# Optimization experiments

Hardware: AMD Instinct MI355X
Metric: run time of the kernel (lower is better)

The kernel has to match this reference:

```python
import jax, jax.numpy as jnp
import numpy as np

B, L, D = 2, 2048, 2048
NH, HD = 16, 128
SCALE = HD ** -0.5


def setup_inputs() -> dict:
    key = jax.random.key(0)
    ks = jax.random.split(key, 9)
    s = D ** -0.5  # roughly torch Linear init scale
    return {
        "hidden_states": jax.random.normal(ks[0], (B, L, D), dtype=jnp.float32),
        "Wq": jax.random.normal(ks[1], (NH * HD, D), dtype=jnp.float32) * s,
        "bq": jnp.zeros((NH * HD,), dtype=jnp.float32),
        "Wk": jax.random.normal(ks[2], (NH * HD, D), dtype=jnp.float32) * s,
        "bk": jnp.zeros((NH * HD,), dtype=jnp.float32),
        "Wv": jax.random.normal(ks[3], (NH * HD, D), dtype=jnp.float32) * s,
        "bv": jnp.zeros((NH * HD,), dtype=jnp.float32),
        "Wo": jax.random.normal(ks[4], (D, NH * HD), dtype=jnp.float32) * s,
        "bo": jnp.zeros((D,), dtype=jnp.float32),
    }


def reference(hidden_states, Wq, bq, Wk, bk, Wv, bv, Wo, bo):
    # projections (torch Linear: x @ W.T + b), split into heads: b s h d
    q = (hidden_states @ Wq.T + bq).reshape(B, L, NH, HD)
    k = (hidden_states @ Wk.T + bk).reshape(B, L, NH, HD)
    v = (hidden_states @ Wv.T + bv).reshape(B, L, NH, HD)
    # scores: [B, NH, L, L]
    scores = jnp.einsum("bqhd,bkhd->bhqk", q, k) * SCALE
    causal = jnp.tril(jnp.ones((L, L), dtype=bool))  # True = keep
    scores = jnp.where(causal, scores, jnp.float32(-jnp.inf))
    probs = jax.nn.softmax(scores, axis=-1)
    out = jnp.einsum("bhqk,bkhd->bqhd", probs, v).reshape(B, L, NH * HD)
    return out @ Wo.T + bo
```

## Files before the change

### kernel.cpp

```cpp
#include <hip/hip_runtime.h>

#define B_  2
#define L_  2048
#define D_  2048
#define NH_ 16
#define HD_ 128

typedef __bf16 bf16_t;
typedef __bf16 bf16x8 __attribute__((ext_vector_type(8)));
typedef __bf16 bf16x4 __attribute__((ext_vector_type(4)));
typedef float  f32x4  __attribute__((ext_vector_type(4)));

typedef const __attribute__((address_space(1))) void* gas_ptr;
typedef __attribute__((address_space(3))) void* las_ptr;

__device__ __forceinline__ void g2l16(const void* g, void* l) {
    __builtin_amdgcn_global_load_lds((gas_ptr)g, (las_ptr)l, 16, 0, 0);
}

__device__ __forceinline__ void raw_barrier() {
    asm volatile("s_barrier" ::: "memory");
}
__device__ __forceinline__ void wait_vm8() {
    asm volatile("s_waitcnt vmcnt(8)" ::: "memory");
}
__device__ __forceinline__ void wait_vm0() {
    asm volatile("s_waitcnt vmcnt(0)" ::: "memory");
}

__global__ __launch_bounds__(256) void cvt_all(const float* __restrict__ X,
                                               const float* __restrict__ Wq,
                                               const float* __restrict__ Wk,
                                               const float* __restrict__ Wv,
                                               const float* __restrict__ Wo,
                                               bf16_t* __restrict__ Xb,
                                               bf16_t* __restrict__ Wqkvb,
                                               bf16_t* __restrict__ Wob) {
    int i = blockIdx.x * 256 + threadIdx.x;
    const float* src;
    bf16_t* dst;
    int off;
    if (i < 2097152) { src = X; dst = Xb; off = i; }
    else {
        int j = i - 2097152;
        int w = j >> 20;
        off = j & 1048575;
        src = (w == 0) ? Wq : (w == 1) ? Wk : (w == 2) ? Wv : Wo;
        dst = (w == 3) ? Wob : Wqkvb + (size_t)w * 4194304;
    }
    float4 v = ((const float4*)src)[off];
    bf16x4 o;
    o[0] = (bf16_t)v.x; o[1] = (bf16_t)v.y; o[2] = (bf16_t)v.z; o[3] = (bf16_t)v.w;
    ((bf16x4*)dst)[off] = o;
}

template <bool BF16OUT>
__global__ __launch_bounds__(256) void gemm_bt(const bf16_t* __restrict__ A,
                                               const bf16_t* __restrict__ Bw,
                                               const float* __restrict__ bias,
                                               void* __restrict__ C,
                                               int M, int N, int K) {
    constexpr int BK = 32;
    __shared__ bf16_t Al[128 * BK];
    __shared__ bf16_t Bl[128 * BK];
    const int tid  = threadIdx.x;
    const int wave = tid >> 6, lane = tid & 63;
    const int quad = lane >> 4, l16 = lane & 15;
    const int tm = blockIdx.y * 128, tn = blockIdx.x * 128;
    const int wm = (wave >> 1) * 64, wn = (wave & 1) * 64;

    const int srow = wave * 16 + (lane >> 2);
    const int scol = (lane & 3) * 8;
    const bf16_t* Ag = A  + (size_t)(tm + srow) * K + scol;
    const bf16_t* Bg = Bw + (size_t)(tn + srow) * K + scol;
    const size_t rowskip = (size_t)64 * K;
    bf16_t* Al0 = Al + (wave * 16) * BK;
    bf16_t* Al1 = Al + (64 + wave * 16) * BK;
    bf16_t* Bl0 = Bl + (wave * 16) * BK;
    bf16_t* Bl1 = Bl + (64 + wave * 16) * BK;

    f32x4 acc[4][4] = {};

    for (int k0 = 0; k0 < K; k0 += BK) {
        g2l16(Ag + k0, Al0);
        g2l16(Ag + k0 + rowskip, Al1);
        g2l16(Bg + k0, Bl0);
        g2l16(Bg + k0 + rowskip, Bl1);
        __syncthreads();

        bf16x8 af[4], bf[4];
#pragma unroll
        for (int i = 0; i < 4; ++i)
            af[i] = *(const bf16x8*)(Al + (wm + i * 16 + l16) * BK + quad * 8);
#pragma unroll
        for (int j = 0; j < 4; ++j)
            bf[j] = *(const bf16x8*)(Bl + (wn + j * 16 + l16) * BK + quad * 8);
#pragma unroll
        for (int i = 0; i < 4; ++i)
#pragma unroll
            for (int j = 0; j < 4; ++j)
                acc[i][j] = __builtin_amdgcn_mfma_f32_16x16x32_bf16(af[i], bf[j], acc[i][j], 0, 0, 0);
        __syncthreads();
    }

#pragma unroll
    for (int j = 0; j < 4; ++j) {
        const int col = tn + wn + j * 16 + l16;
        const float bv = bias[col];
#pragma unroll
        for (int i = 0; i < 4; ++i) {
            const int row0 = tm + wm + i * 16 + quad * 4;
#pragma unroll
            for (int r = 0; r < 4; ++r) {
                float v = acc[i][j][r] + bv;
                if (BF16OUT)
                    ((bf16_t*)C)[(size_t)(row0 + r) * N + col] = (bf16_t)v;
                else
                    ((float*)C)[(size_t)(row0 + r) * N + col] = v;
            }
        }
    }
}

__global__ __launch_bounds__(256) void gemm_qkv(const bf16_t* __restrict__ A,
                                                const bf16_t* __restrict__ Bw,
                                                const float* __restrict__ b0,
                                                const float* __restrict__ b1,
                                                const float* __restrict__ b2,
                                                bf16_t* __restrict__ C,
                                                int M, int N, int K) {
    constexpr int BK = 32;
    __shared__ bf16_t Al[128 * BK];
    __shared__ bf16_t Bl[128 * BK];
    const int tid  = threadIdx.x;
    const int wave = tid >> 6, lane = tid & 63;
    const int quad = lane >> 4, l16 = lane & 15;
    const int tm = blockIdx.y * 128, tn = blockIdx.x * 128;
    const int wm = (wave >> 1) * 64, wn = (wave & 1) * 64;

    const int seg = tn >> 11;
    const float* bias = (seg == 0) ? b0 : (seg == 1) ? b1 : b2;

    const int srow = wave * 16 + (lane >> 2);
    const int scol = (lane & 3) * 8;
    const bf16_t* Ag = A  + (size_t)(tm + srow) * K + scol;
    const bf16_t* Bg = Bw + (size_t)(tn + srow) * K + scol;
    const size_t rowskip = (size_t)64 * K;
    bf16_t* Al0 = Al + (wave * 16) * BK;
    bf16_t* Al1 = Al + (64 + wave * 16) * BK;
    bf16_t* Bl0 = Bl + (wave * 16) * BK;
    bf16_t* Bl1 = Bl + (64 + wave * 16) * BK;

    f32x4 acc[4][4] = {};

    for (int k0 = 0; k0 < K; k0 += BK) {
        g2l16(Ag + k0, Al0);
        g2l16(Ag + k0 + rowskip, Al1);
        g2l16(Bg + k0, Bl0);
        g2l16(Bg + k0 + rowskip, Bl1);
        __syncthreads();

        bf16x8 af[4], bf[4];
#pragma unroll
        for (int i = 0; i < 4; ++i)
            af[i] = *(const bf16x8*)(Al + (wm + i * 16 + l16) * BK + quad * 8);
#pragma unroll
        for (int j = 0; j < 4; ++j)
            bf[j] = *(const bf16x8*)(Bl + (wn + j * 16 + l16) * BK + quad * 8);
#pragma unroll
        for (int i = 0; i < 4; ++i)
#pragma unroll
            for (int j = 0; j < 4; ++j)
                acc[i][j] = __builtin_amdgcn_mfma_f32_16x16x32_bf16(af[i], bf[j], acc[i][j], 0, 0, 0);
        __syncthreads();
    }

#pragma unroll
    for (int j = 0; j < 4; ++j) {
        const int col = tn + wn + j * 16 + l16;
        const float bv = bias[col & 2047];
#pragma unroll
        for (int i = 0; i < 4; ++i) {
            const int row0 = tm + wm + i * 16 + quad * 4;
#pragma unroll
            for (int r = 0; r < 4; ++r)
                C[(size_t)(row0 + r) * N + col] = (bf16_t)(acc[i][j][r] + bv);
        }
    }
}

__global__ __launch_bounds__(256) void transpose_v(const bf16_t* __restrict__ QKV,
                                                   bf16_t* __restrict__ Vt) {
    __shared__ bf16_t t[64 * 136];
    const int tid = threadIdx.x;
    const int tt = blockIdx.x;
    const int bh = blockIdx.y;
    const int b = bh >> 4, h = bh & 15;
#pragma unroll
    for (int c = 0; c < 8; ++c) {
        int chunk = c * 256 + tid;
        int tok = chunk >> 5;
        int dof = (chunk & 31) * 4;
        bf16x4 v = *(const bf16x4*)(QKV + (size_t)(b * L_ + tt * 64 + tok) * 6144 + 4096 + h * HD_ + dof);
        *(bf16x4*)(&t[tok * 136 + dof]) = v;
    }
    __syncthreads();
#pragma unroll
    for (int c = 0; c < 4; ++c) {
        int chunk = c * 256 + tid;
        int d = chunk >> 3;
        int tof = (chunk & 7) * 8;
        bf16x8 v;
#pragma unroll
        for (int j = 0; j < 8; ++j) v[j] = t[(tof + j) * 136 + d];
        *(bf16x8*)(Vt + (size_t)(bh * HD_ + d) * L_ + tt * 64 + tof) = v;
    }
}

__global__ __launch_bounds__(256, 2) void attn_kernel(const bf16_t* __restrict__ QKV,
                                                      const bf16_t* __restrict__ Vt,
                                                      bf16_t* __restrict__ Ctx) {
    constexpr float SCALE = 0.08838834764831845f;
    constexpr float MFIX  = 8.0f;
    const int bid = blockIdx.x;
    const int bh = bid & 31;
    const int qt = 15 - (bid >> 5);
    const int b = bh >> 4, h = bh & 15;
    const int tid = threadIdx.x, wave = tid >> 6, lane = tid & 63;
    const int quad = lane >> 4, l16 = lane & 15;
    const int q0 = qt * 128;

    __shared__ bf16_t Kl[2][64 * 128];
    __shared__ bf16_t Vl[2][128 * 64];
    __shared__ bf16_t Pl[4][16 * 72];

    bf16x8 qf[2][4];
#pragma unroll
    for (int s = 0; s < 2; ++s) {
        const bf16_t* qp = QKV + (size_t)(b * L_ + q0 + wave * 32 + s * 16 + l16) * 6144 + h * HD_ + quad * 8;
#pragma unroll
        for (int ks = 0; ks < 4; ++ks) qf[s][ks] = *(const bf16x8*)(qp + ks * 32);
    }

    bf16x8 ones;
#pragma unroll
    for (int j = 0; j < 8; ++j) ones[j] = (bf16_t)1.0f;

    f32x4 oacc[2][8] = {};
    f32x4 lacc[2] = {};

    const bf16_t* Kg = QKV + (size_t)(b * L_) * 6144 + 2048 + h * HD_;
    const bf16_t* Vg = Vt + (size_t)(bh * HD_) * L_;

    auto stage = [&](int tile, int p) {
        const bf16_t* kg = Kg + (size_t)tile * 64 * 6144;
        const bf16_t* vg = Vg + tile * 64;
#pragma unroll
        for (int c = 0; c < 4; ++c) {
            int row = c * 16 + wave * 4 + (lane >> 4);
            int gcol = ((lane & 15) ^ (row & 15)) * 8;
            g2l16(kg + (size_t)row * 6144 + gcol, &Kl[p][(c * 16 + wave * 4) * 128]);
        }
#pragma unroll
        for (int c = 0; c < 4; ++c) {
            int row = c * 32 + wave * 8 + (lane >> 3);
            int gcol = ((lane & 7) ^ (row & 7)) * 8;
            g2l16(vg + (size_t)row * L_ + gcol, &Vl[p][(c * 32 + wave * 8) * 64]);
        }
    };

    const int n = 2 * qt + 2;
    stage(0, 0);

    for (int it = 0; it < n; ++it) {
        const int p = it & 1;
        if (it + 1 < n) {
            stage(it + 1, p ^ 1);
            wait_vm8();
        } else {
            wait_vm0();
        }
        raw_barrier();

        const int kb = it * 64;
        const bool need_mask = (it >= n - 2);

        f32x4 sa[2][4] = {};
#pragma unroll
        for (int nt = 0; nt < 4; ++nt) {
            const int krow = nt * 16 + l16;
#pragma unroll
            for (int ks = 0; ks < 4; ++ks) {
                bf16x8 kf = *(const bf16x8*)(&Kl[p][krow * 128 + (((ks * 4 + quad) ^ l16) * 8)]);
                sa[0][nt] = __builtin_amdgcn_mfma_f32_16x16x32_bf16(qf[0][ks], kf, sa[0][nt], 0, 0, 0);
                sa[1][nt] = __builtin_amdgcn_mfma_f32_16x16x32_bf16(qf[1][ks], kf, sa[1][nt], 0, 0, 0);
            }
        }

        bf16x8 pf0[2], pf1[2];
#pragma unroll
        for (int nt = 0; nt < 4; ++nt)
#pragma unroll
            for (int r = 0; r < 4; ++r) {
                float sv = sa[0][nt][r] * SCALE - MFIX;
                if (need_mask) {
                    const int key = kb + nt * 16 + l16;
                    const int qq = q0 + wave * 32 + quad * 4 + r;
                    sv = (key <= qq) ? sv : -1e30f;
                }
                Pl[wave][(quad * 4 + r) * 72 + nt * 16 + l16] = (bf16_t)__expf(sv);
            }
        pf0[0] = *(const bf16x8*)(&Pl[wave][l16 * 72 + quad * 8]);
        pf0[1] = *(const bf16x8*)(&Pl[wave][l16 * 72 + 32 + quad * 8]);

#pragma unroll
        for (int nt = 0; nt < 4; ++nt)
#pragma unroll
            for (int r = 0; r < 4; ++r) {
                float sv = sa[1][nt][r] * SCALE - MFIX;
                if (need_mask) {
                    const int key = kb + nt * 16 + l16;
                    const int qq = q0 + wave * 32 + 16 + quad * 4 + r;
                    sv = (key <= qq) ? sv : -1e30f;
                }
                Pl[wave][(quad * 4 + r) * 72 + nt * 16 + l16] = (bf16_t)__expf(sv);
            }
        pf1[0] = *(const bf16x8*)(&Pl[wave][l16 * 72 + quad * 8]);
        pf1[1] = *(const bf16x8*)(&Pl[wave][l16 * 72 + 32 + quad * 8]);

        lacc[0] = __builtin_amdgcn_mfma_f32_16x16x32_bf16(pf0[0], ones, lacc[0], 0, 0, 0);
        lacc[0] = __builtin_amdgcn_mfma_f32_16x16x32_bf16(pf0[1], ones, lacc[0], 0, 0, 0);
        lacc[1] = __builtin_amdgcn_mfma_f32_16x16x32_bf16(pf1[0], ones, lacc[1], 0, 0, 0);
        lacc[1] = __builtin_amdgcn_mfma_f32_16x16x32_bf16(pf1[1], ones, lacc[1], 0, 0, 0);

#pragma unroll
        for (int dt = 0; dt < 8; ++dt) {
            const int drow = dt * 16 + l16;
#pragma unroll
            for (int ks = 0; ks < 2; ++ks) {
                bf16x8 vf = *(const bf16x8*)(&Vl[p][drow * 64 + (((ks * 4 + quad) ^ (drow & 7)) * 8)]);
                oacc[0][dt] = __builtin_amdgcn_mfma_f32_16x16x32_bf16(pf0[ks], vf, oacc[0][dt], 0, 0, 0);
                oacc[1][dt] = __builtin_amdgcn_mfma_f32_16x16x32_bf16(pf1[ks], vf, oacc[1][dt], 0, 0, 0);
            }
        }
        raw_barrier();
    }

#pragma unroll
    for (int s = 0; s < 2; ++s)
#pragma unroll
        for (int r = 0; r < 4; ++r) {
            const float inv = 1.0f / lacc[s][r];
            const int q = q0 + wave * 32 + s * 16 + quad * 4 + r;
            bf16_t* cp = Ctx + (size_t)(b * L_ + q) * 2048 + h * HD_;
#pragma unroll
            for (int dt = 0; dt < 8; ++dt)
                cp[dt * 16 + l16] = (bf16_t)(oacc[s][dt][r] * inv);
        }
}

extern "C" void kernel_launch(void* const* d_in, const int* in_sizes, int n_in,
                              void* d_out, int out_size, void* d_ws, size_t ws_size,
                              hipStream_t stream) {
    const float* X  = (const float*)d_in[0];
    const float* Wq = (const float*)d_in[1];
    const float* bq = (const float*)d_in[2];
    const float* Wk = (const float*)d_in[3];
    const float* bk = (const float*)d_in[4];
    const float* Wv = (const float*)d_in[5];
    const float* bv = (const float*)d_in[6];
    const float* Wo = (const float*)d_in[7];
    const float* bo = (const float*)d_in[8];
    float* out = (float*)d_out;

    char* ws = (char*)d_ws;
    bf16_t* Xb   = (bf16_t*)(ws);
    bf16_t* Vtb  = (bf16_t*)(ws);
    bf16_t* Wqkv = (bf16_t*)(ws + 16777216);
    bf16_t* Ctx  = (bf16_t*)(ws + 16777216);
    bf16_t* Wob  = (bf16_t*)(ws + 41943040);
    bf16_t* QKV  = (bf16_t*)(ws + 50331648);

    cvt_all<<<24576, 256, 0, stream>>>(X, Wq, Wk, Wv, Wo, Xb, Wqkv, Wob);

    gemm_qkv<<<dim3(48, 32), 256, 0, stream>>>(Xb, Wqkv, bq, bk, bv, QKV,
                                               B_ * L_, 3 * D_, D_);

    transpose_v<<<dim3(L_ / 64, B_ * NH_), 256, 0, stream>>>(QKV, Vtb);
    attn_kernel<<<dim3(512), 256, 0, stream>>>(QKV, Vtb, Ctx);

    gemm_bt<false><<<dim3(16, 32), 256, 0, stream>>>(Ctx, Wob, bo, out,
                                                     B_ * L_, D_, D_);
}
```

Measured before the change: 409.2 us.

## Double-buffer GEMM LDS loads and fuse V transpose into QKV GEMM epilogue

Both GEMM kernels now use a two-stage LDS buffer. The next K-tile's global-to-LDS loads are issued before computing the current one, with vmcnt waits and raw barriers replacing the per-iteration syncthreads, so memory latency is meant to overlap with MFMA work. The QKV GEMM's V-segment blocks write a transposed V through a swizzled LDS tile straight into the Vt layout, which removes the separate transpose kernel and its extra pass over V. Q and K now go to a narrower 4096-wide buffer, and the workspace layout changes to match. The trade-off is doubled LDS use, which may lower occupancy.

```diff
diff --git a/kernel.cpp b/kernel.cpp
--- a/kernel.cpp
+++ b/kernel.cpp
@@ -23,6 +23,9 @@
 }
 __device__ __forceinline__ void wait_vm8() {
     asm volatile("s_waitcnt vmcnt(8)" ::: "memory");
+}
+__device__ __forceinline__ void wait_vm4() {
+    asm volatile("s_waitcnt vmcnt(4)" ::: "memory");
 }
 __device__ __forceinline__ void wait_vm0() {
     asm volatile("s_waitcnt vmcnt(0)" ::: "memory");
@@ -54,15 +57,13 @@
     ((bf16x4*)dst)[off] = o;
 }
 
-template <bool BF16OUT>
 __global__ __launch_bounds__(256) void gemm_bt(const bf16_t* __restrict__ A,
                                                const bf16_t* __restrict__ Bw,
                                                const float* __restrict__ bias,
-                                               void* __restrict__ C,
+                                               float* __restrict__ C,
                                                int M, int N, int K) {
     constexpr int BK = 32;
-    __shared__ bf16_t Al[128 * BK];
-    __shared__ bf16_t Bl[128 * BK];
+    __shared__ __align__(16) bf16_t smem[16384];
     const int tid  = threadIdx.x;
     const int wave = tid >> 6, lane = tid & 63;
     const int quad = lane >> 4, l16 = lane & 15;
@@ -74,33 +75,41 @@
     const bf16_t* Ag = A  + (size_t)(tm + srow) * K + scol;
     const bf16_t* Bg = Bw + (size_t)(tn + srow) * K + scol;
     const size_t rowskip = (size_t)64 * K;
-    bf16_t* Al0 = Al + (wave * 16) * BK;
-    bf16_t* Al1 = Al + (64 + wave * 16) * BK;
-    bf16_t* Bl0 = Bl + (wave * 16) * BK;
-    bf16_t* Bl1 = Bl + (64 + wave * 16) * BK;
+
+    auto stage = [&](int k0, int p) {
+        bf16_t* a = smem + p * 4096 + (wave * 16) * BK;
+        bf16_t* bl = smem + 8192 + p * 4096 + (wave * 16) * BK;
+        g2l16(Ag + k0, a);
+        g2l16(Ag + k0 + rowskip, a + 64 * BK);
+        g2l16(Bg + k0, bl);
+        g2l16(Bg + k0 + rowskip, bl + 64 * BK);
+    };
 
     f32x4 acc[4][4] = {};
-
-    for (int k0 = 0; k0 < K; k0 += BK) {
-        g2l16(Ag + k0, Al0);
-        g2l16(Ag + k0 + rowskip, Al1);
-        g2l16(Bg + k0, Bl0);
-        g2l16(Bg + k0 + rowskip, Bl1);
-        __syncthreads();
-
+    const int niter = K / BK;
+    stage(0, 0);
+
+    for (int i = 0; i < niter; ++i) {
+        const int p = i & 1;
+        if (i + 1 < niter) { stage((i + 1) * BK, p ^ 1); wait_vm4(); }
+        else wait_vm0();
+        raw_barrier();
+
+        const bf16_t* Alp = smem + p * 4096;
+        const bf16_t* Blp = smem + 8192 + p * 4096;
         bf16x8 af[4], bf[4];
 #pragma unroll
-        for (int i = 0; i < 4; ++i)
-            af[i] = *(const bf16x8*)(Al + (wm + i * 16 + l16) * BK + quad * 8);
+        for (int ii = 0; ii < 4; ++ii)
+            af[ii] = *(const bf16x8*)(Alp + (wm + ii * 16 + l16) * BK + quad * 8);
 #pragma unroll
         for (int j = 0; j < 4; ++j)
-            bf[j] = *(const bf16x8*)(Bl + (wn + j * 16 + l16) * BK + quad * 8);
-#pragma unroll
-        for (int i = 0; i < 4; ++i)
+            bf[j] = *(const bf16x8*)(Blp + (wn + j * 16 + l16) * BK + quad * 8);
+#pragma unroll
+        for (int ii = 0; ii < 4; ++ii)
 #pragma unroll
             for (int j = 0; j < 4; ++j)
-                acc[i][j] = __builtin_amdgcn_mfma_f32_16x16x32_bf16(af[i], bf[j], acc[i][j], 0, 0, 0);
-        __syncthreads();
+                acc[ii][j] = __builtin_amdgcn_mfma_f32_16x16x32_bf16(af[ii], bf[j], acc[ii][j], 0, 0, 0);
+        raw_barrier();
     }
 
 #pragma unroll
@@ -111,13 +120,8 @@
         for (int i = 0; i < 4; ++i) {
             const int row0 = tm + wm + i * 16 + quad * 4;
 #pragma unroll
-            for (int r = 0; r < 4; ++r) {
-                float v = acc[i][j][r] + bv;
-                if (BF16OUT)
-                    ((bf16_t*)C)[(size_t)(row0 + r) * N + col] = (bf16_t)v;
-                else
-                    ((float*)C)[(size_t)(row0 + r) * N + col] = v;
-            }
+            for (int r = 0; r < 4; ++r)
+                C[(size_t)(row0 + r) * N + col] = acc[i][j][r] + bv;
         }
     }
 }
@@ -127,11 +131,10 @@
                                                 const float* __restrict__ b0,
                                                 const float* __restrict__ b1,
                                                 const float* __restrict__ b2,
-                                                bf16_t* __restrict__ C,
-                                                int M, int N, int K) {
-    constexpr int BK = 32;
-    __shared__ bf16_t Al[128 * BK];
-    __shared__ bf16_t Bl[128 * BK];
+                                                bf16_t* __restrict__ QK,
+                                                bf16_t* __restrict__ Vt) {
+    constexpr int BK = 32, K = D_;
+    __shared__ __align__(16) bf16_t smem[17408];
     const int tid  = threadIdx.x;
     const int wave = tid >> 6, lane = tid & 63;
     const int quad = lane >> 4, l16 = lane & 15;
@@ -146,78 +149,87 @@
     const bf16_t* Ag = A  + (size_t)(tm + srow) * K + scol;
     const bf16_t* Bg = Bw + (size_t)(tn + srow) * K + scol;
     const size_t rowskip = (size_t)64 * K;
-    bf16_t* Al0 = Al + (wave * 16) * BK;
-    bf16_t* Al1 = Al + (64 + wave * 16) * BK;
-    bf16_t* Bl0 = Bl + (wave * 16) * BK;
-    bf16_t* Bl1 = Bl + (64 + wave * 16) * BK;
+
+    auto stage = [&](int k0, int p) {
+        bf16_t* a = smem + p * 4096 + (wave * 16) * BK;
+        bf16_t* bl = smem + 8192 + p * 4096 + (wave * 16) * BK;
+        g2l16(Ag + k0, a);
+        g2l16(Ag + k0 + rowskip, a + 64 * BK);
+        g2l16(Bg + k0, bl);
+        g2l16(Bg + k0 + rowskip, bl + 64 * BK);
+    };
 
     f32x4 acc[4][4] = {};
-
-    for (int k0 = 0; k0 < K; k0 += BK) {
-        g2l16(Ag + k0, Al0);
-        g2l16(Ag + k0 + rowskip, Al1);
-        g2l16(Bg + k0, Bl0);
-        g2l16(Bg + k0 + rowskip, Bl1);
+    const int niter = K / BK;
+    stage(0, 0);
+
+    for (int i = 0; i < niter; ++i) {
+        const int p = i & 1;
+        if (i + 1 < niter) { stage((i + 1) * BK, p ^ 1); wait_vm4(); }
+        else wait_vm0();
+        raw_barrier();
+
+        const bf16_t* Alp = smem + p * 4096;
+        const bf16_t* Blp = smem + 8192 + p * 4096;
+        bf16x8 af[4], bf[4];
+#pragma unroll
+        for (int ii = 0; ii < 4; ++ii)
+            af[ii] = *(const bf16x8*)(Alp + (wm + ii * 16 + l16) * BK + quad * 8);
+#pragma unroll
+        for (int j = 0; j < 4; ++j)
+            bf[j] = *(const bf16x8*)(Blp + (wn + j * 16 + l16) * BK + quad * 8);
+#pragma unroll
+        for (int ii = 0; ii < 4; ++ii)
+#pragma unroll
+            for (int j = 0; j < 4; ++j)
+                acc[ii][j] = __builtin_amdgcn_mfma_f32_16x16x32_bf16(af[ii], bf[j], acc[ii][j], 0, 0, 0);
+        raw_barrier();
+    }
+
+    if (seg < 2) {
+#pragma unroll
+        for (int j = 0; j < 4; ++j) {
+            const int col = tn + wn + j * 16 + l16;
+            const float bv = bias[col & 2047];
+#pragma unroll
+            for (int i = 0; i < 4; ++i) {
+                const int row0 = tm + wm + i * 16 + quad * 4;
+#pragma unroll
+                for (int r = 0; r < 4; ++r)
+                    QK[(size_t)(row0 + r) * 4096 + col] = (bf16_t)(acc[i][j][r] + bv);
+            }
+        }
+    } else {
+        const int h = (tn >> 7) - 32;
+        const int b = tm >> 11;
+        const int tokbase = tm & 2047;
         __syncthreads();
-
-        bf16x8 af[4], bf[4];
-#pragma unroll
-        for (int i = 0; i < 4; ++i)
-            af[i] = *(const bf16x8*)(Al + (wm + i * 16 + l16) * BK + quad * 8);
-#pragma unroll
-        for (int j = 0; j < 4; ++j)
-            bf[j] = *(const bf16x8*)(Bl + (wn + j * 16 + l16) * BK + quad * 8);
-#pragma unroll
-        for (int i = 0; i < 4; ++i)
-#pragma unroll
-            for (int j = 0; j < 4; ++j)
-                acc[i][j] = __builtin_amdgcn_mfma_f32_16x16x32_bf16(af[i], bf[j], acc[i][j], 0, 0, 0);
+#pragma unroll
+        for (int j = 0; j < 4; ++j) {
+            const int d = wn + j * 16 + l16;
+            const float bv = bias[(tn + wn + j * 16 + l16) & 2047];
+#pragma unroll
+            for (int i = 0; i < 4; ++i)
+#pragma unroll
+                for (int r = 0; r < 4; ++r) {
+                    const int tok = wm + i * 16 + quad * 4 + r;
+                    smem[d * 136 + (((tok >> 3) ^ (d & 7)) << 3) + (tok & 7)] =
+                        (bf16_t)(acc[i][j][r] + bv);
+                }
+        }
         __syncthreads();
-    }
-
-#pragma unroll
-    for (int j = 0; j < 4; ++j) {
-        const int col = tn + wn + j * 16 + l16;
-        const float bv = bias[col & 2047];
-#pragma unroll
-        for (int i = 0; i < 4; ++i) {
-            const int row0 = tm + wm + i * 16 + quad * 4;
-#pragma unroll
-            for (int r = 0; r < 4; ++r)
-                C[(size_t)(row0 + r) * N + col] = (bf16_t)(acc[i][j][r] + bv);
-        }
-    }
-}
-
-__global__ __launch_bounds__(256) void transpose_v(const bf16_t* __restrict__ QKV,
-                                                   bf16_t* __restrict__ Vt) {
-    __shared__ bf16_t t[64 * 136];
-    const int tid = threadIdx.x;
-    const int tt = blockIdx.x;
-    const int bh = blockIdx.y;
-    const int b = bh >> 4, h = bh & 15;
-#pragma unroll
-    for (int c = 0; c < 8; ++c) {
-        int chunk = c * 256 + tid;
-        int tok = chunk >> 5;
-        int dof = (chunk & 31) * 4;
-        bf16x4 v = *(const bf16x4*)(QKV + (size_t)(b * L_ + tt * 64 + tok) * 6144 + 4096 + h * HD_ + dof);
-        *(bf16x4*)(&t[tok * 136 + dof]) = v;
-    }
-    __syncthreads();
-#pragma unroll
-    for (int c = 0; c < 4; ++c) {
-        int chunk = c * 256 + tid;
-        int d = chunk >> 3;
-        int tof = (chunk & 7) * 8;
-        bf16x8 v;
-#pragma unroll
-        for (int j = 0; j < 8; ++j) v[j] = t[(tof + j) * 136 + d];
-        *(bf16x8*)(Vt + (size_t)(bh * HD_ + d) * L_ + tt * 64 + tof) = v;
-    }
-}
-
-__global__ __launch_bounds__(256, 2) void attn_kernel(const bf16_t* __restrict__ QKV,
+        const int d = tid >> 1, half = tid & 1;
+        bf16_t* gp = Vt + ((size_t)(b * NH_ + h) * HD_ + d) * L_ + tokbase + half * 64;
+#pragma unroll
+        for (int c2 = 0; c2 < 8; ++c2) {
+            const int cc = half * 8 + c2;
+            bf16x8 v = *(const bf16x8*)(smem + d * 136 + ((cc ^ (d & 7)) << 3));
+            *(bf16x8*)(gp + c2 * 8) = v;
+        }
+    }
+}
+
+__global__ __launch_bounds__(256, 2) void attn_kernel(const bf16_t* __restrict__ QK,
                                                       const bf16_t* __restrict__ Vt,
                                                       bf16_t* __restrict__ Ctx) {
     constexpr float SCALE = 0.08838834764831845f;
@@ -237,7 +249,7 @@
     bf16x8 qf[2][4];
 #pragma unroll
     for (int s = 0; s < 2; ++s) {
-        const bf16_t* qp = QKV + (size_t)(b * L_ + q0 + wave * 32 + s * 16 + l16) * 6144 + h * HD_ + quad * 8;
+        const bf16_t* qp = QK + (size_t)(b * L_ + q0 + wave * 32 + s * 16 + l16) * 4096 + h * HD_ + quad * 8;
 #pragma unroll
         for (int ks = 0; ks < 4; ++ks) qf[s][ks] = *(const bf16x8*)(qp + ks * 32);
     }
@@ -249,17 +261,17 @@
     f32x4 oacc[2][8] = {};
     f32x4 lacc[2] = {};
 
-    const bf16_t* Kg = QKV + (size_t)(b * L_) * 6144 + 2048 + h * HD_;
+    const bf16_t* Kg = QK + (size_t)(b * L_) * 4096 + 2048 + h * HD_;
     const bf16_t* Vg = Vt + (size_t)(bh * HD_) * L_;
 
     auto stage = [&](int tile, int p) {
-        const bf16_t* kg = Kg + (size_t)tile * 64 * 6144;
+        const bf16_t* kg = Kg + (size_t)tile * 64 * 4096;
         const bf16_t* vg = Vg + tile * 64;
 #pragma unroll
         for (int c = 0; c < 4; ++c) {
             int row = c * 16 + wave * 4 + (lane >> 4);
             int gcol = ((lane & 15) ^ (row & 15)) * 8;
-            g2l16(kg + (size_t)row * 6144 + gcol, &Kl[p][(c * 16 + wave * 4) * 128]);
+            g2l16(kg + (size_t)row * 4096 + gcol, &Kl[p][(c * 16 + wave * 4) * 128]);
         }
 #pragma unroll
         for (int c = 0; c < 4; ++c) {
@@ -375,20 +387,18 @@
 
     char* ws = (char*)d_ws;
     bf16_t* Xb   = (bf16_t*)(ws);
-    bf16_t* Vtb  = (bf16_t*)(ws);
+    bf16_t* Ctx  = (bf16_t*)(ws);
     bf16_t* Wqkv = (bf16_t*)(ws + 16777216);
-    bf16_t* Ctx  = (bf16_t*)(ws + 16777216);
     bf16_t* Wob  = (bf16_t*)(ws + 41943040);
-    bf16_t* QKV  = (bf16_t*)(ws + 50331648);
+    bf16_t* QKb  = (bf16_t*)(ws + 50331648);
+    bf16_t* Vtb  = (bf16_t*)(ws + 83886080);
 
     cvt_all<<<24576, 256, 0, stream>>>(X, Wq, Wk, Wv, Wo, Xb, Wqkv, Wob);
 
-    gemm_qkv<<<dim3(48, 32), 256, 0, stream>>>(Xb, Wqkv, bq, bk, bv, QKV,
-                                               B_ * L_, 3 * D_, D_);
-
-    transpose_v<<<dim3(L_ / 64, B_ * NH_), 256, 0, stream>>>(QKV, Vtb);
-    attn_kernel<<<dim3(512), 256, 0, stream>>>(QKV, Vtb, Ctx);
-
-    gemm_bt<false><<<dim3(16, 32), 256, 0, stream>>>(Ctx, Wob, bo, out,
-                                                     B_ * L_, D_, D_);
-}
+    gemm_qkv<<<dim3(48, 32), 256, 0, stream>>>(Xb, Wqkv, bq, bk, bv, QKb, Vtb);
+
+    attn_kernel<<<dim3(512), 256, 0, stream>>>(QKb, Vtb, Ctx);
+
+    gemm_bt<<<dim3(16, 32), 256, 0, stream>>>(Ctx, Wob, bo, out,
+                                              B_ * L_, D_, D_);
+}
```

After: 378.0 us. 1.08x faster.
